# Performance work log

Hardware: AMD Instinct MI355X
Metric: run time of the kernel (lower is better)

## Reference

```python
import jax, jax.numpy as jnp
import numpy as np

K_SIZE = 5
PAD = 2  # (dilation*(k-1)+1 - stride + 1)//2 with k=5, dil=1, stride=1
SAMPLE_NUM = 15
DEPTH_MAX = 192.0


def _gather_patches(x, sample_idx):
    """x: [B,C,H,W] -> [B,H,W,S,C]: values of the 5x5 local neighborhood at the
    SAMPLE_NUM sampled kernel positions (zero padding, matching nn.Unfold)."""
    B, C, H, W = x.shape
    xp = jnp.pad(x, ((0, 0), (0, 0), (PAD, PAD), (PAD, PAD)))
    slabs = []
    for i in range(SAMPLE_NUM):  # small fixed constant, not a data dim
        p = sample_idx[i]
        dy = p // K_SIZE
        dx = p % K_SIZE
        slabs.append(jax.lax.dynamic_slice(xp, (0, 0, dy, dx), (B, C, H, W)))
    pat = jnp.stack(slabs, axis=1)          # [B,S,C,H,W]
    return pat.transpose(0, 3, 4, 1, 2)     # [B,H,W,S,C]


def setup_inputs() -> dict:
    key = jax.random.key(0)
    k1, k2, k3, k4 = jax.random.split(key, 4)
    B, C, H, W = 2, 32, 240, 320
    depth = jax.random.uniform(k1, (B, 1, H, W), dtype=jnp.float32) * 200.0
    surface_normal = jax.random.normal(k2, (B, 3, H, W), dtype=jnp.float32)
    features = jax.random.normal(k3, (B, C, H, W), dtype=jnp.float32)
    guide_weight = jnp.ones((B, H, W, K_SIZE * K_SIZE), dtype=jnp.float32)
    sample_idx = jax.random.randint(k4, (SAMPLE_NUM,), 0, K_SIZE * K_SIZE, dtype=jnp.int32)
    return {"depth": depth, "surface_normal": surface_normal, "features": features,
            "guide_weight": guide_weight, "sample_idx": sample_idx}


def reference(depth, surface_normal, features, guide_weight, sample_idx):
    b, c, h, w = features.shape
    d = depth[:, 0]                                          # squeeze(1) -> [B,H,W]
    valid = ((d > 0) & (d < DEPTH_MAX)).astype(features.dtype)[:, None]  # [B,1,H,W]

    feat_s = _gather_patches(features, sample_idx)           # [B,H,W,S,C]
    norm_s = _gather_patches(surface_normal, sample_idx)     # [B,H,W,S,3]
    valid_s = _gather_patches(valid, sample_idx)[..., 0]     # [B,H,W,S]

    # Faithful to torch: surface_normal.view(b, h, w, 3) is a raw memory
    # reinterpretation, NOT a permute.
    center_n = jnp.reshape(surface_normal, (b, h, w, 3))
    diff = jnp.sqrt(jnp.sum((norm_s - center_n[:, :, :, None, :]) ** 2, axis=-1))
    # torch detaches via the cpu/numpy round-trip -> stop_gradient here
    normal_w = jax.lax.stop_gradient(jnp.exp(-0.5 * diff))   # [B,H,W,S]

    guide_s = jnp.take(guide_weight, sample_idx, axis=3)     # [B,H,W,S]

    fw = valid_s * normal_w * guide_s                        # both weight flags True
    fw = jax.nn.softmax(fw, axis=-1)
    out = jnp.sum(feat_s * fw[..., None], axis=3)            # [B,H,W,C]
    return (out.transpose(0, 3, 1, 2), features)
```

## Files before the change

kernel.cpp:

```cpp
#include <hip/hip_runtime.h>

#define K_SIZE 5
#define PAD 2
#define SAMPLE_NUM 15
#define DEPTH_MAX 192.0f

constexpr int B = 2, C = 32, H = 240, W = 320;
constexpr int HW = H * W;
constexpr int BHW = B * HW;
constexpr size_t WS_NEED = (size_t)BHW * 16 * sizeof(float);

__global__ __launch_bounds__(256) void weights_kernel(
    const float* __restrict__ depth,
    const float* __restrict__ sn,
    const float* __restrict__ guide,
    const int*   __restrict__ sample_idx,
    float* __restrict__ wpre)
{
    const int t   = threadIdx.x;
    const int s   = t & 15;
    const int lp  = t >> 4;
    const int pg  = blockIdx.x * 16 + lp;
    const int b   = pg / HW;
    const int pix = pg - b * HW;
    const int y   = pix / W;
    const int x   = pix - y * W;

    const float* snb = sn + (size_t)b * 3 * HW;
    const float* db  = depth + (size_t)b * HW;

    float ww = 0.0f;
    if (s < SAMPLE_NUM) {
        int o = y * (W * 3) + x * 3;
        float cn0 = snb[o], cn1 = snb[o + 1], cn2 = snb[o + 2];

        int pp = sample_idx[s];
        int dy = pp / K_SIZE - PAD;
        int dx = pp - (pp / K_SIZE) * K_SIZE - PAD;
        int yy = y + dy, xx = x + dx;
        bool inb = (yy >= 0) && (yy < H) && (xx >= 0) && (xx < W);
        ww = -1.0f;
        if (inb) {
            ww = 0.0f;
            int noff = yy * W + xx;
            float d = db[noff];
            if (d > 0.0f && d < DEPTH_MAX) {
                float d0 = snb[noff]          - cn0;
                float d1 = snb[HW + noff]     - cn1;
                float d2 = snb[2 * HW + noff] - cn2;
                float diff = sqrtf(d0 * d0 + d1 * d1 + d2 * d2);
                ww = __expf(-0.5f * diff) * guide[((size_t)b * HW + pix) * 25 + pp];
            }
        }
    }
    wpre[(size_t)pg * 16 + s] = ww;
}

constexpr int NGB = 8, CPGB = 4;
constexpr int PB_BLOCKS = BHW / 256;
constexpr int XCD_CHUNK = PB_BLOCKS / 8;

__global__ __launch_bounds__(256) void gather_kernel(
    const float* __restrict__ features,
    const int*   __restrict__ sample_idx,
    const float* __restrict__ wpre,
    float* __restrict__ out,
    float* __restrict__ feat_out)
{
    int bid = blockIdx.x;
    int xcd = bid & 7;
    int k   = bid >> 3;
    int pb  = xcd * XCD_CHUNK + (k % XCD_CHUNK);
    int g   = k / XCD_CHUNK;

    const int t   = threadIdx.x;
    const int pg  = pb * 256 + t;
    const int b   = pg / HW;
    const int pix = pg - b * HW;
    const int y   = pix / W;
    const int x   = pix - y * W;

    const float4* wp = (const float4*)(wpre + (size_t)pg * 16);
    float4 q0 = wp[0], q1 = wp[1], q2 = wp[2], q3 = wp[3];
    float v[16] = {q0.x, q0.y, q0.z, q0.w, q1.x, q1.y, q1.z, q1.w,
                   q2.x, q2.y, q2.z, q2.w, q3.x, q3.y, q3.z, q3.w};

    int offs[SAMPLE_NUM];
    #pragma unroll
    for (int s = 0; s < SAMPLE_NUM; ++s) {
        int pp = sample_idx[s];
        int dy = pp / K_SIZE - PAD;
        int dx = pp - (pp / K_SIZE) * K_SIZE - PAD;
        int yy = y + dy, xx = x + dx;
        bool inb = (yy >= 0) && (yy < H) && (xx >= 0) && (xx < W);
        offs[s] = inb ? (yy * W + xx) : pix;
    }

    float m = 0.0f;
    #pragma unroll
    for (int s = 0; s < SAMPLE_NUM; ++s) m = fmaxf(m, v[s]);
    float e[SAMPLE_NUM];
    float sum = 0.0f;
    #pragma unroll
    for (int s = 0; s < SAMPLE_NUM; ++s) {
        e[s] = __expf(fmaxf(v[s], 0.0f) - m);
        sum += e[s];
    }
    float inv = 1.0f / sum;
    float wv[SAMPLE_NUM];
    #pragma unroll
    for (int s = 0; s < SAMPLE_NUM; ++s)
        wv[s] = (v[s] < 0.0f) ? 0.0f : e[s] * inv;

    const float* fb  = features + (size_t)b * C * HW;
    float*       ob  = out      + (size_t)b * C * HW;
    float*       fob = feat_out + (size_t)b * C * HW;
    const int c0 = g * CPGB;

    float acc[CPGB];
    #pragma unroll
    for (int cc = 0; cc < CPGB; ++cc) acc[cc] = 0.0f;

    #pragma unroll
    for (int s = 0; s < SAMPLE_NUM; ++s) {
        const float* fo = fb + offs[s];
        float wgt = wv[s];
        #pragma unroll
        for (int cc = 0; cc < CPGB; ++cc)
            acc[cc] = fmaf(wgt, fo[(size_t)(c0 + cc) * HW], acc[cc]);
    }

    #pragma unroll
    for (int cc = 0; cc < CPGB; ++cc) {
        size_t idx = (size_t)(c0 + cc) * HW + pix;
        ob[idx]  = acc[cc];
        fob[idx] = fb[idx];
    }
}

__global__ __launch_bounds__(256) void fused_fallback(
    const float* __restrict__ depth, const float* __restrict__ sn,
    const float* __restrict__ features, const float* __restrict__ guide,
    const int* __restrict__ sample_idx, float* __restrict__ out,
    float* __restrict__ feat_out)
{
    constexpr int PIX_BLOCKS = BHW / 256;
    int pb = blockIdx.x % PIX_BLOCKS;
    int g  = blockIdx.x / PIX_BLOCKS;
    int n  = pb * 256 + threadIdx.x;
    int b = n / HW, pix = n - b * HW, y = pix / W, x = pix - y * W;
    const float* snb = sn + (size_t)b * 3 * HW;
    const float* db  = depth + (size_t)b * HW;
    const float* gb  = guide + ((size_t)b * HW + pix) * 25;
    int o = y * (W * 3) + x * 3;
    float cn0 = snb[o], cn1 = snb[o + 1], cn2 = snb[o + 2];
    float w[SAMPLE_NUM]; int offs[SAMPLE_NUM]; bool inbv[SAMPLE_NUM];
    float m = 0.0f;
    #pragma unroll
    for (int s = 0; s < SAMPLE_NUM; ++s) {
        int pp = sample_idx[s];
        int dy = pp / K_SIZE - PAD, dx = pp - (pp / K_SIZE) * K_SIZE - PAD;
        int yy = y + dy, xx = x + dx;
        bool inb = (yy >= 0) && (yy < H) && (xx >= 0) && (xx < W);
        inbv[s] = inb;
        int noff = inb ? (yy * W + xx) : pix;
        offs[s] = noff;
        float ww = 0.0f;
        if (inb) {
            float d = db[noff];
            if (d > 0.0f && d < DEPTH_MAX) {
                float d0 = snb[noff] - cn0, d1 = snb[HW + noff] - cn1, d2 = snb[2 * HW + noff] - cn2;
                ww = __expf(-0.5f * sqrtf(d0 * d0 + d1 * d1 + d2 * d2)) * gb[pp];
            }
        }
        w[s] = ww; m = fmaxf(m, ww);
    }
    float sum = 0.0f;
    #pragma unroll
    for (int s = 0; s < SAMPLE_NUM; ++s) { w[s] = __expf(w[s] - m); sum += w[s]; }
    float inv = 1.0f / sum;
    #pragma unroll
    for (int s = 0; s < SAMPLE_NUM; ++s) w[s] = inbv[s] ? (w[s] * inv) : 0.0f;
    const float* fb = features + (size_t)b * C * HW;
    float* ob = out + (size_t)b * C * HW;
    float* fob = feat_out + (size_t)b * C * HW;
    int c0 = g * 8;
    #pragma unroll
    for (int cc = 0; cc < 8; ++cc) {
        const float* fc = fb + (c0 + cc) * HW;
        float acc = 0.0f;
        #pragma unroll
        for (int s = 0; s < SAMPLE_NUM; ++s) acc += w[s] * fc[offs[s]];
        ob[(size_t)(c0 + cc) * HW + pix] = acc;
        fob[(size_t)(c0 + cc) * HW + pix] = fc[pix];
    }
}

extern "C" void kernel_launch(void* const* d_in, const int* in_sizes, int n_in,
                              void* d_out, int out_size, void* d_ws, size_t ws_size,
                              hipStream_t stream) {
    const float* depth      = (const float*)d_in[0];
    const float* sn         = (const float*)d_in[1];
    const float* features   = (const float*)d_in[2];
    const float* guide      = (const float*)d_in[3];
    const int*   sample_idx = (const int*)d_in[4];

    float* out      = (float*)d_out;
    float* feat_out = (float*)d_out + (size_t)B * C * HW;

    if (ws_size >= WS_NEED) {
        float* wpre = (float*)d_ws;
        weights_kernel<<<BHW / 16, 256, 0, stream>>>(depth, sn, guide, sample_idx, wpre);
        gather_kernel<<<PB_BLOCKS * NGB, 256, 0, stream>>>(features, sample_idx, wpre, out, feat_out);
    } else {
        fused_fallback<<<(BHW / 256) * 4, 256, 0, stream>>>(
            depth, sn, features, guide, sample_idx, out, feat_out);
    }
}
```

Measured before the change: 42.12 us.

## Move softmax into weights kernel and vectorize gather over four pixels per thread

The weights kernel now computes the softmax across the 16 sample lanes with width-16 shuffles. It writes normalized weights in a sample-major [S][BHW] layout instead of the per-pixel 16-wide pre-weights. The gather kernel has each thread handle four consecutive pixels of one channel, using float4 loads of weights and unaligned float4 feature row loads, and vector stores for the output and feature copy. This is meant to cut redundant per-channel-group softmax work and scalar gathers, at the cost of boundary scalar paths and unaligned vector loads.

```diff
diff --git a/kernel.cpp b/kernel.cpp
--- a/kernel.cpp
+++ b/kernel.cpp
@@ -8,14 +8,17 @@
 constexpr int B = 2, C = 32, H = 240, W = 320;
 constexpr int HW = H * W;
 constexpr int BHW = B * HW;
-constexpr size_t WS_NEED = (size_t)BHW * 16 * sizeof(float);
+constexpr size_t WS_NEED = (size_t)SAMPLE_NUM * BHW * sizeof(float);
+
+typedef float float4a __attribute__((ext_vector_type(4), aligned(16)));
+typedef float float4u __attribute__((ext_vector_type(4), aligned(4)));
 
 __global__ __launch_bounds__(256) void weights_kernel(
     const float* __restrict__ depth,
     const float* __restrict__ sn,
     const float* __restrict__ guide,
     const int*   __restrict__ sample_idx,
-    float* __restrict__ wpre)
+    float* __restrict__ wpost)
 {
     const int t   = threadIdx.x;
     const int s   = t & 15;
@@ -29,113 +32,99 @@
     const float* snb = sn + (size_t)b * 3 * HW;
     const float* db  = depth + (size_t)b * HW;
 
-    float ww = 0.0f;
+    float prew = 0.0f;
+    bool  inb  = false;
     if (s < SAMPLE_NUM) {
-        int o = y * (W * 3) + x * 3;
-        float cn0 = snb[o], cn1 = snb[o + 1], cn2 = snb[o + 2];
-
         int pp = sample_idx[s];
         int dy = pp / K_SIZE - PAD;
         int dx = pp - (pp / K_SIZE) * K_SIZE - PAD;
         int yy = y + dy, xx = x + dx;
-        bool inb = (yy >= 0) && (yy < H) && (xx >= 0) && (xx < W);
-        ww = -1.0f;
+        inb = (yy >= 0) && (yy < H) && (xx >= 0) && (xx < W);
         if (inb) {
-            ww = 0.0f;
             int noff = yy * W + xx;
             float d = db[noff];
             if (d > 0.0f && d < DEPTH_MAX) {
+                int o = pix * 3;
+                float cn0 = snb[o], cn1 = snb[o + 1], cn2 = snb[o + 2];
                 float d0 = snb[noff]          - cn0;
                 float d1 = snb[HW + noff]     - cn1;
                 float d2 = snb[2 * HW + noff] - cn2;
                 float diff = sqrtf(d0 * d0 + d1 * d1 + d2 * d2);
-                ww = __expf(-0.5f * diff) * guide[((size_t)b * HW + pix) * 25 + pp];
+                prew = __expf(-0.5f * diff) * guide[((size_t)b * HW + pix) * 25 + pp];
             }
         }
     }
-    wpre[(size_t)pg * 16 + s] = ww;
-}
-
-constexpr int NGB = 8, CPGB = 4;
-constexpr int PB_BLOCKS = BHW / 256;
-constexpr int XCD_CHUNK = PB_BLOCKS / 8;
+
+    float m = prew;
+    #pragma unroll
+    for (int mask = 1; mask < 16; mask <<= 1)
+        m = fmaxf(m, __shfl_xor(m, mask, 16));
+    float e = (s < SAMPLE_NUM) ? __expf(prew - m) : 0.0f;
+    float sum = e;
+    #pragma unroll
+    for (int mask = 1; mask < 16; mask <<= 1)
+        sum += __shfl_xor(sum, mask, 16);
+
+    if (s < SAMPLE_NUM)
+        wpost[(size_t)s * BHW + pg] = inb ? (e / sum) : 0.0f;
+}
+
+constexpr int CHUNKS = BHW / 256;
+constexpr int XCHUNK = CHUNKS / 8;
 
 __global__ __launch_bounds__(256) void gather_kernel(
     const float* __restrict__ features,
     const int*   __restrict__ sample_idx,
-    const float* __restrict__ wpre,
+    const float* __restrict__ wpost,
     float* __restrict__ out,
     float* __restrict__ feat_out)
 {
-    int bid = blockIdx.x;
-    int xcd = bid & 7;
-    int k   = bid >> 3;
-    int pb  = xcd * XCD_CHUNK + (k % XCD_CHUNK);
-    int g   = k / XCD_CHUNK;
+    int bid   = blockIdx.x;
+    int xcd   = bid & 7;
+    int k     = bid >> 3;
+    int chunk = xcd * XCHUNK + (k % XCHUNK);
+    int g     = k / XCHUNK;
 
     const int t   = threadIdx.x;
-    const int pg  = pb * 256 + t;
-    const int b   = pg / HW;
-    const int pix = pg - b * HW;
-    const int y   = pix / W;
-    const int x   = pix - y * W;
-
-    const float4* wp = (const float4*)(wpre + (size_t)pg * 16);
-    float4 q0 = wp[0], q1 = wp[1], q2 = wp[2], q3 = wp[3];
-    float v[16] = {q0.x, q0.y, q0.z, q0.w, q1.x, q1.y, q1.z, q1.w,
-                   q2.x, q2.y, q2.z, q2.w, q3.x, q3.y, q3.z, q3.w};
-
-    int offs[SAMPLE_NUM];
+    const int qc  = t & 63;
+    const int cs  = t >> 6;
+    const int c   = g * 4 + cs;
+    const int pg0 = chunk * 256 + qc * 4;
+    const int b   = pg0 / HW;
+    const int pix0 = pg0 - b * HW;
+    const int y   = pix0 / W;
+    const int x0  = pix0 - y * W;
+
+    const float* fb = features + ((size_t)b * C + c) * HW;
+
+    float4a acc = {0.0f, 0.0f, 0.0f, 0.0f};
+
     #pragma unroll
     for (int s = 0; s < SAMPLE_NUM; ++s) {
         int pp = sample_idx[s];
         int dy = pp / K_SIZE - PAD;
         int dx = pp - (pp / K_SIZE) * K_SIZE - PAD;
-        int yy = y + dy, xx = x + dx;
-        bool inb = (yy >= 0) && (yy < H) && (xx >= 0) && (xx < W);
-        offs[s] = inb ? (yy * W + xx) : pix;
-    }
-
-    float m = 0.0f;
-    #pragma unroll
-    for (int s = 0; s < SAMPLE_NUM; ++s) m = fmaxf(m, v[s]);
-    float e[SAMPLE_NUM];
-    float sum = 0.0f;
-    #pragma unroll
-    for (int s = 0; s < SAMPLE_NUM; ++s) {
-        e[s] = __expf(fmaxf(v[s], 0.0f) - m);
-        sum += e[s];
-    }
-    float inv = 1.0f / sum;
-    float wv[SAMPLE_NUM];
-    #pragma unroll
-    for (int s = 0; s < SAMPLE_NUM; ++s)
-        wv[s] = (v[s] < 0.0f) ? 0.0f : e[s] * inv;
-
-    const float* fb  = features + (size_t)b * C * HW;
-    float*       ob  = out      + (size_t)b * C * HW;
-    float*       fob = feat_out + (size_t)b * C * HW;
-    const int c0 = g * CPGB;
-
-    float acc[CPGB];
-    #pragma unroll
-    for (int cc = 0; cc < CPGB; ++cc) acc[cc] = 0.0f;
-
-    #pragma unroll
-    for (int s = 0; s < SAMPLE_NUM; ++s) {
-        const float* fo = fb + offs[s];
-        float wgt = wv[s];
-        #pragma unroll
-        for (int cc = 0; cc < CPGB; ++cc)
-            acc[cc] = fmaf(wgt, fo[(size_t)(c0 + cc) * HW], acc[cc]);
-    }
-
-    #pragma unroll
-    for (int cc = 0; cc < CPGB; ++cc) {
-        size_t idx = (size_t)(c0 + cc) * HW + pix;
-        ob[idx]  = acc[cc];
-        fob[idx] = fb[idx];
-    }
+        int yy = y + dy;
+        if (yy < 0 || yy >= H) continue;
+        float4a w4 = *(const float4a*)(wpost + (size_t)s * BHW + pg0);
+        const float* frow = fb + yy * W;
+        int xx0 = x0 + dx;
+        if (xx0 >= 0 && xx0 <= W - 4) {
+            float4u f4 = *(const float4u*)(frow + xx0);
+            acc += w4 * f4;
+        } else {
+            #pragma unroll
+            for (int i = 0; i < 4; ++i) {
+                int xx = xx0 + i;
+                if (xx >= 0 && xx < W) acc[i] += w4[i] * frow[xx];
+            }
+        }
+    }
+
+    size_t obase = ((size_t)b * C + c) * HW + pix0;
+    float4a pf = *(const float4a*)(fb + pix0);
+    *(float4a*)(out + obase)      = acc;
+    *(float4a*)(feat_out + obase) = pf;
 }
 
 __global__ __launch_bounds__(256) void fused_fallback(
@@ -152,7 +141,7 @@
     const float* snb = sn + (size_t)b * 3 * HW;
     const float* db  = depth + (size_t)b * HW;
     const float* gb  = guide + ((size_t)b * HW + pix) * 25;
-    int o = y * (W * 3) + x * 3;
+    int o = pix * 3;
     float cn0 = snb[o], cn1 = snb[o + 1], cn2 = snb[o + 2];
     float w[SAMPLE_NUM]; int offs[SAMPLE_NUM]; bool inbv[SAMPLE_NUM];
     float m = 0.0f;
@@ -209,9 +198,9 @@
     float* feat_out = (float*)d_out + (size_t)B * C * HW;
 
     if (ws_size >= WS_NEED) {
-        float* wpre = (float*)d_ws;
-        weights_kernel<<<BHW / 16, 256, 0, stream>>>(depth, sn, guide, sample_idx, wpre);
-        gather_kernel<<<PB_BLOCKS * NGB, 256, 0, stream>>>(features, sample_idx, wpre, out, feat_out);
+        float* wpost = (float*)d_ws;
+        weights_kernel<<<BHW / 16, 256, 0, stream>>>(depth, sn, guide, sample_idx, wpost);
+        gather_kernel<<<CHUNKS * 8, 256, 0, stream>>>(features, sample_idx, wpost, out, feat_out);
     } else {
         fused_fallback<<<(BHW / 256) * 4, 256, 0, stream>>>(
             depth, sn, features, guide, sample_idx, out, feat_out);
```

Result: slower. 59.09 us (+40.3%).
